# Performance work log

Hardware: AMD Instinct MI355X
Metric: run time of the kernel (lower is better)

The kernel has to match this reference:

```python
import jax, jax.numpy as jnp
import numpy as np

DIM = 512
NUM_LATENTS = 512
HIDDEN = 48  # PointEmbed sinusoidal embedding dim (divisible by 6)


def make_basis():
    k = HIDDEN // 6
    e = (2.0 ** np.arange(k)) * np.pi
    z = np.zeros(k)
    basis = np.stack([
        np.concatenate([e, z, z]),
        np.concatenate([z, e, z]),
        np.concatenate([z, z, e]),
    ])  # [3, HIDDEN//2]
    return jnp.asarray(basis, jnp.float32)


def layernorm(x, g, b, eps=1e-5):
    m = x.mean(-1, keepdims=True)
    v = ((x - m) ** 2).mean(-1, keepdims=True)
    return (x - m) / jnp.sqrt(v + eps) * g + b


def point_embed(x, basis, w, b):
    # x: [B, N, 3] -> [B, N, DIM//2]
    proj = jnp.einsum('bnd,de->bne', x, basis)
    feat = jnp.concatenate([jnp.sin(proj), jnp.cos(proj), x], axis=-1)  # [B,N,51]
    return feat @ w + b


def fps_single(points, num_samples):
    # deterministic farthest point sampling starting at index 0; non-differentiable
    pts = jax.lax.stop_gradient(points)
    N = pts.shape[0]

    def body(carry, _):
        dists, last = carry
        d = jnp.sum((pts - pts[last]) ** 2, axis=-1)
        dists = jnp.minimum(dists, d)
        nxt = jnp.argmax(dists).astype(jnp.int32)
        return (dists, nxt), nxt

    init = (jnp.full((N,), 1e10, pts.dtype), jnp.int32(0))
    _, idxs = jax.lax.scan(body, init, None, length=num_samples - 1)
    return jnp.concatenate([jnp.zeros((1,), jnp.int32), idxs])


def setup_inputs() -> dict:
    key = jax.random.key(0)
    ks = jax.random.split(key, 16)
    B, T, N, D = 16, 3, 2048, 3
    s = 0.02
    inp = {
        'pc': jax.random.normal(ks[0], (B, T, N, D), jnp.float32),
        'pc2': jax.random.normal(ks[1], (B, T, N, D), jnp.float32),
        'basis': make_basis(),
        'pe_w': jax.random.normal(ks[2], (HIDDEN + 3, DIM // 2), jnp.float32) * s,
        'pe_b': jnp.zeros((DIM // 2,), jnp.float32),
        'lnq_g': jnp.ones((DIM,), jnp.float32), 'lnq_b': jnp.zeros((DIM,), jnp.float32),
        'lnc_g': jnp.ones((DIM,), jnp.float32), 'lnc_b': jnp.zeros((DIM,), jnp.float32),
        'wq': jax.random.normal(ks[3], (DIM, DIM), jnp.float32) * s,
        'wkv': jax.random.normal(ks[4], (DIM, 2 * DIM), jnp.float32) * s,
        'wo': jax.random.normal(ks[5], (DIM, DIM), jnp.float32) * s,
        'bo': jnp.zeros((DIM,), jnp.float32),
        'lnf_g': jnp.ones((DIM,), jnp.float32), 'lnf_b': jnp.zeros((DIM,), jnp.float32),
        'w1': jax.random.normal(ks[6], (DIM, 8 * DIM), jnp.float32) * s,
        'b1': jnp.zeros((8 * DIM,), jnp.float32),
        'w2': jax.random.normal(ks[7], (4 * DIM, DIM), jnp.float32) * s,
        'b2': jnp.zeros((DIM,), jnp.float32),
    }
    return inp


def reference(pc, pc2, basis, pe_w, pe_b, lnq_g, lnq_b, lnc_g, lnc_b,
              wq, wkv, wo, bo, lnf_g, lnf_b, w1, b1, w2, b2):
    B, T, N, D = pc.shape
    # FPS on the first frame, per batch element (batch-local indices)
    idx = jax.vmap(lambda p: fps_single(p, NUM_LATENTS))(pc[:, 0])  # [B, M]
    idx4 = idx[:, None, :, None]  # broadcast over T and D
    sampled = jnp.take_along_axis(pc, idx4, axis=2).reshape(B * T, NUM_LATENTS, D)
    sampled2 = jnp.take_along_axis(pc2, idx4, axis=2).reshape(B * T, NUM_LATENTS, D)
    pcf = pc.reshape(B * T, N, D)
    pcf2 = pc2.reshape(B * T, N, D)

    emb_s = jnp.concatenate([point_embed(sampled, basis, pe_w, pe_b),
                             point_embed(sampled2, basis, pe_w, pe_b)], axis=-1)
    emb_c = jnp.concatenate([point_embed(pcf, basis, pe_w, pe_b),
                             point_embed(pcf2, basis, pe_w, pe_b)], axis=-1)

    # PreNorm cross-attention (1 head, dim_head = DIM)
    q_in = layernorm(emb_s, lnq_g, lnq_b)
    c_in = layernorm(emb_c, lnc_g, lnc_b)
    q = q_in @ wq
    kv = c_in @ wkv
    k, v = jnp.split(kv, 2, axis=-1)
    scale = DIM ** -0.5
    attn = jax.nn.softmax(jnp.einsum('bmd,bnd->bmn', q, k) * scale, axis=-1)
    out = jnp.einsum('bmn,bnd->bmd', attn, v) @ wo + bo
    x = out + emb_s

    # PreNorm GEGLU feed-forward
    h = layernorm(x, lnf_g, lnf_b) @ w1 + b1
    a, g = jnp.split(h, 2, axis=-1)
    x = (a * jax.nn.gelu(g, approximate=False)) @ w2 + b2 + x

    return x.reshape(B, T, NUM_LATENTS, DIM)
```

## Files before the change

kernel.cpp:

```cpp
#include <hip/hip_runtime.h>

#define NB    16
#define NT    3
#define NCTX  2048
#define NLAT  512
#define DIMV  512
#define HALFD 256
#define NFEAT 51
#define NBT   48
#define MROWS 24576
#define GRP   6
#define NGRP  8
#define GROWS 12288

typedef unsigned short bfu;
typedef short bf16x8 __attribute__((ext_vector_type(8)));
typedef float f32x4  __attribute__((ext_vector_type(4)));
typedef float f32x2  __attribute__((ext_vector_type(2)));

__device__ __forceinline__ float bf2f(bfu u){ return __uint_as_float(((unsigned int)u) << 16); }
__device__ __forceinline__ bfu f2bf(float f){
  unsigned int u = __float_as_uint(f);
  u += 0x7FFFu + ((u >> 16) & 1u);
  return (bfu)(u >> 16);
}
__device__ __forceinline__ float loadE(const float* p){ return *p; }
__device__ __forceinline__ float loadE(const bfu* p){ return bf2f(*p); }
__device__ __forceinline__ void storeE(float* p, float v){ *p = v; }
__device__ __forceinline__ void storeE(bfu* p, float v){ *p = f2bf(v); }
__device__ __forceinline__ bfu to_bfu(float f){ return f2bf(f); }
__device__ __forceinline__ bfu to_bfu(bfu u){ return u; }

#define GLD16(gp, lp) __builtin_amdgcn_global_load_lds(                       \
    (const __attribute__((address_space(1))) unsigned int*)(gp),              \
    (__attribute__((address_space(3))) unsigned int*)(lp), 16, 0, 0)

template<int KSTEP>
__device__ __forceinline__ int swzr(int r){
  constexpr int CPR = KSTEP / 8;
  return (KSTEP == 32) ? ((r >> 1) & 3) : (r & (CPR - 1));
}

#define DPP_ARGMAX_STAGE(CTRL)                                                \
  {                                                                           \
    const int svb = __builtin_amdgcn_update_dpp(vb, vb, CTRL, 0xF, 0xF, false); \
    const int sib = __builtin_amdgcn_update_dpp(ib, ib, CTRL, 0xF, 0xF, false); \
    const float sv = __int_as_float(svb);                                     \
    const float cv = __int_as_float(vb);                                      \
    if (sv > cv || (sv == cv && sib < ib)){ vb = svb; ib = sib; }             \
  }

__global__ __attribute__((amdgpu_waves_per_eu(1, 1)))
__launch_bounds__(128) void fps_kernel(const float* __restrict__ pc,
                                       int* __restrict__ idx_out){
#pragma clang fp contract(off)
  __shared__ float4 pts[NCTX];
  __shared__ __align__(16) int mbuf[2][4];
  const int tid = threadIdx.x;
  const int lane = tid & 63, w = tid >> 6;
  const int wbase = w << 10;
  const int b = blockIdx.x;
  const float* src = pc + (size_t)b * (NT * NCTX * 3);

  f32x2 x2[8], y2[8], z2[8], d2[8];
  #pragma unroll
  for (int j = 0; j < 8; ++j){
    #pragma unroll
    for (int h = 0; h < 2; ++h){
      const int p = wbase + ((2 * j + h) << 6) + lane;
      const float xx = src[p * 3 + 0];
      const float yy = src[p * 3 + 1];
      const float zz = src[p * 3 + 2];
      x2[j][h] = xx; y2[j][h] = yy; z2[j][h] = zz;
      pts[p] = make_float4(xx, yy, zz, 0.f);
    }
    d2[j][0] = 1e10f; d2[j][1] = 1e10f;
  }
  if (tid == 0) idx_out[b * NLAT] = 0;
  __syncthreads();

  int last = 0;
  for (int step = 1; step < NLAT; ++step){
    const float4 lp = pts[last];

    #pragma unroll
    for (int j = 0; j < 8; ++j){
      const f32x2 dx = x2[j] - lp.x;
      const f32x2 dy = y2[j] - lp.y;
      const f32x2 dz = z2[j] - lp.z;
      const f32x2 dd = (dx * dx + dy * dy) + dz * dz;
      f32x2 nd;
      nd[0] = fminf(d2[j][0], dd[0]);
      nd[1] = fminf(d2[j][1], dd[1]);
      d2[j] = nd;
    }

    float av[8]; int as_[8];
    #pragma unroll
    for (int j = 0; j < 8; ++j){
      const float lo = d2[j][0], hi = d2[j][1];
      const bool t = hi > lo;
      av[j]  = t ? hi : lo;
      as_[j] = t ? 2 * j + 1 : 2 * j;
    }
    #pragma unroll
    for (int wdt = 4; wdt; wdt >>= 1){
      #pragma unroll
      for (int j = 0; j < wdt; ++j){
        const float lv = av[2 * j], rv = av[2 * j + 1];
        const int   li = as_[2 * j], ri = as_[2 * j + 1];
        const bool t = rv > lv;
        av[j]  = t ? rv : lv;
        as_[j] = t ? ri : li;
      }
    }

    int vb = __float_as_int(av[0]);
    int ib = wbase + (as_[0] << 6) + lane;
    DPP_ARGMAX_STAGE(0x111)
    DPP_ARGMAX_STAGE(0x112)
    DPP_ARGMAX_STAGE(0x114)
    DPP_ARGMAX_STAGE(0x118)
    DPP_ARGMAX_STAGE(0x142)
    DPP_ARGMAX_STAGE(0x143)

    const int par = step & 1;
    if (lane == 63){ mbuf[par][w * 2] = vb; mbuf[par][w * 2 + 1] = ib; }
    __syncthreads();
    const int4 q = *(const int4*)&mbuf[par][0];
    const float f0 = __int_as_float(q.x), f1 = __int_as_float(q.z);
    last = (f1 > f0) ? q.w : q.y;
    if (tid == 0) idx_out[b * NLAT + step] = last;
  }
}

template<bool GATHER, bool WRITE_EMB>
__global__ __launch_bounds__(256) void embed_kernel(
    const float* __restrict__ pc, const float* __restrict__ pc2,
    const int* __restrict__ idx,
    const float* __restrict__ basis, const float* __restrict__ pe_w,
    const float* __restrict__ pe_b,
    const float* __restrict__ ln_g, const float* __restrict__ ln_b,
    bfu* __restrict__ emb, bfu* __restrict__ lnout, int nppbt)
{
  __shared__ float feat[2][16][NFEAT + 1];
  __shared__ float outb[16][DIMV];
  const int tid = threadIdx.x;
  const int p0 = blockIdx.x << 4;

  if (tid < 32){
    const int s = tid >> 4, p = tid & 15;
    const int gp = p0 + p;
    const int bt = gp / nppbt;
    const int n  = gp - bt * nppbt;
    const int bb = bt / NT;
    const int srcn = GATHER ? idx[bb * NLAT + n] : n;
    const float* sp = (s ? pc2 : pc) + ((size_t)bt * NCTX + srcn) * 3;
    const float x0 = sp[0], x1 = sp[1], x2 = sp[2];
    #pragma unroll
    for (int e = 0; e < 24; ++e){
      const float pr = __fadd_rn(__fadd_rn(__fmul_rn(x0, basis[e]),
                                           __fmul_rn(x1, basis[24 + e])),
                                 __fmul_rn(x2, basis[48 + e]));
      feat[s][p][e]      = sinf(pr);
      feat[s][p][24 + e] = cosf(pr);
    }
    feat[s][p][48] = x0; feat[s][p][49] = x1; feat[s][p][50] = x2;
  }
  __syncthreads();

  {
    float w[NFEAT];
    #pragma unroll
    for (int k = 0; k < NFEAT; ++k) w[k] = pe_w[k * HALFD + tid];
    const float bv = pe_b[tid];
    #pragma unroll
    for (int half = 0; half < 2; ++half){
      for (int p = 0; p < 16; ++p){
        float acc = bv;
        #pragma unroll
        for (int k = 0; k < NFEAT; ++k) acc = fmaf(feat[half][p][k], w[k], acc);
        outb[p][half * HALFD + tid] = acc;
      }
    }
  }
  __syncthreads();

  const int lane = tid & 63, wv = tid >> 6;
  for (int pp = 0; pp < 4; ++pp){
    const int p = (wv << 2) + pp;
    const size_t gp = (size_t)p0 + p;
    float x[8];
    #pragma unroll
    for (int j = 0; j < 8; ++j) x[j] = outb[p][lane + (j << 6)];
    float s = 0.f;
    #pragma unroll
    for (int j = 0; j < 8; ++j) s += x[j];
    for (int o = 32; o; o >>= 1) s += __shfl_xor(s, o, 64);
    const float m = s * (1.0f / 512.0f);
    float s2 = 0.f;
    #pragma unroll
    for (int j = 0; j < 8; ++j){ const float d = x[j] - m; s2 = fmaf(d, d, s2); }
    for (int o = 32; o; o >>= 1) s2 += __shfl_xor(s2, o, 64);
    const float inv = 1.0f / sqrtf(s2 * (1.0f / 512.0f) + 1e-5f);
    #pragma unroll
    for (int j = 0; j < 8; ++j){
      const int c = lane + (j << 6);
      const float r = (x[j] - m) * inv * ln_g[c] + ln_b[c];
      const size_t o2 = gp * DIMV + c;
      if (WRITE_EMB) emb[o2] = f2bf(x[j]);
      lnout[o2] = f2bf(r);
    }
  }
}

template<typename TIN>
__global__ __launch_bounds__(256) void transp_kernel(
    const TIN* __restrict__ in, bfu* __restrict__ out, int R, int C,
    long long sIn, long long sOut)
{
  __shared__ bfu t[32][33];
  in  += (size_t)blockIdx.z * sIn;
  out += (size_t)blockIdx.z * sOut;
  const int c0 = blockIdx.x * 32, r0 = blockIdx.y * 32;
  const int tx = threadIdx.x & 31, ty = threadIdx.x >> 5;
  #pragma unroll
  for (int rr = ty; rr < 32; rr += 8)
    t[rr][tx] = to_bfu(in[(size_t)(r0 + rr) * C + c0 + tx]);
  __syncthreads();
  #pragma unroll
  for (int rr = ty; rr < 32; rr += 8)
    out[(size_t)(c0 + rr) * R + r0 + tx] = t[tx][rr];
}

#define EPI_NONE     0
#define EPI_SPLIT    1
#define EPI_SCALE    2
#define EPI_BIAS_RES 3

template<int FH, int KSTEP, typename TC, typename TR, int EPI>
__global__ __launch_bounds__(256, 2) void gemm_mfma(
    const bfu* __restrict__ A, const bfu* __restrict__ B,
    TC* __restrict__ C, TC* __restrict__ C2,
    const float* __restrict__ bias, const TR* __restrict__ res,
    float scale, int N, int K, int lda, int ldb, int ldc,
    long long sA, long long sB, long long sC)
{
  constexpr int BT  = FH * 32;
  constexpr int CPR = KSTEP / 8;
  constexpr int NI  = (BT * CPR) / 256;
  const int bz = blockIdx.z;
  A += (size_t)bz * sA;
  B += (size_t)bz * sB;
  const size_t coff = (size_t)bz * sC;

  __shared__ __align__(16) short As[BT * KSTEP];
  __shared__ __align__(16) short Bs[BT * KSTEP];

  const int tid = threadIdx.x;
  const int lane = tid & 63, w = tid >> 6;
  const int wl = (w << 6) + lane;
  const int m0 = blockIdx.y * BT, n0 = blockIdx.x * BT;
  const int wm = (w & 1) * (FH * 16), wn = (w >> 1) * (FH * 16);
  const int fr = lane & 15, quad = lane >> 4;

  f32x4 acc[FH][FH];
  #pragma unroll
  for (int i = 0; i < FH; ++i)
    #pragma unroll
    for (int j = 0; j < FH; ++j)
      #pragma unroll
      for (int r = 0; r < 4; ++r) acc[i][j][r] = 0.f;

  for (int k0 = 0; k0 < K; k0 += KSTEP){
    #pragma unroll
    for (int i = 0; i < NI; ++i){
      const int ch = i * 256 + wl;
      const int r  = ch / CPR, cs = ch & (CPR - 1);
      const int cg = cs ^ swzr<KSTEP>(r);
      short* la = (short*)As + ((i * 256 + (w << 6)) << 3);
      short* lb = (short*)Bs + ((i * 256 + (w << 6)) << 3);
      GLD16(A + (size_t)(m0 + r) * lda + k0 + cg * 8, la);
      GLD16(B + (size_t)(n0 + r) * ldb + k0 + cg * 8, lb);
    }
    __syncthreads();
    #pragma unroll
    for (int kk = 0; kk < KSTEP / 32; ++kk){
      bf16x8 af[FH], bf[FH];
      #pragma unroll
      for (int i = 0; i < FH; ++i){
        const int row = wm + i * 16 + fr;
        const int cl = (kk * 4 + quad) ^ swzr<KSTEP>(row);
        af[i] = *(const bf16x8*)&As[row * KSTEP + (cl << 3)];
      }
      #pragma unroll
      for (int j = 0; j < FH; ++j){
        const int row = wn + j * 16 + fr;
        const int cl = (kk * 4 + quad) ^ swzr<KSTEP>(row);
        bf[j] = *(const bf16x8*)&Bs[row * KSTEP + (cl << 3)];
      }
      #pragma unroll
      for (int i = 0; i < FH; ++i)
        #pragma unroll
        for (int j = 0; j < FH; ++j)
          acc[i][j] = __builtin_amdgcn_mfma_f32_16x16x32_bf16(af[i], bf[j], acc[i][j], 0, 0, 0);
    }
    __syncthreads();
  }

  TC* Cp = C + coff;
  #pragma unroll
  for (int i = 0; i < FH; ++i){
    #pragma unroll
    for (int r = 0; r < 4; ++r){
      const int cm = m0 + wm + i * 16 + quad * 4 + r;
      #pragma unroll
      for (int j = 0; j < FH; ++j){
        const int cn = n0 + wn + j * 16 + fr;
        float v = acc[i][j][r];
        if (EPI == EPI_SCALE)    v *= scale;
        if (EPI == EPI_BIAS_RES) v = v + bias[cn] + loadE(&res[coff + (size_t)cm * ldc + cn]);
        if (EPI == EPI_SPLIT){
          const int half = N >> 1;
          if (cn < half) storeE(&C [(size_t)cm * half + cn],          v);
          else           storeE(&C2[(size_t)cm * half + (cn - half)], v);
        } else {
          storeE(&Cp[(size_t)cm * ldc + cn], v);
        }
      }
    }
  }
}

__global__ __launch_bounds__(256, 1) void mlp1_mfma(
    const bfu* __restrict__ A, const bfu* __restrict__ B,
    const float* __restrict__ b1, bfu* __restrict__ act)
{
  constexpr int KSTEP = 64, CPR = 8, NI = 4;
  __shared__ __align__(16) short As[128 * KSTEP];
  __shared__ __align__(16) short Ba[128 * KSTEP];
  __shared__ __align__(16) short Bg[128 * KSTEP];

  const int tid = threadIdx.x;
  const int lane = tid & 63, w = tid >> 6;
  const int wl = (w << 6) + lane;
  const int m0 = blockIdx.y * 128, n0 = blockIdx.x * 128;
  const int wm = (w & 1) * 64, wn = (w >> 1) * 64;
  const int fr = lane & 15, quad = lane >> 4;

  f32x4 acca[4][4], accg[4][4];
  #pragma unroll
  for (int i = 0; i < 4; ++i)
    #pragma unroll
    for (int j = 0; j < 4; ++j)
      #pragma unroll
      for (int r = 0; r < 4; ++r){ acca[i][j][r] = 0.f; accg[i][j][r] = 0.f; }

  for (int k0 = 0; k0 < 512; k0 += KSTEP){
    #pragma unroll
    for (int i = 0; i < NI; ++i){
      const int ch = i * 256 + wl;
      const int r  = ch / CPR, cs = ch & (CPR - 1);
      const int cg = cs ^ swzr<KSTEP>(r);
      short* da = (short*)As + ((i * 256 + (w << 6)) << 3);
      short* db = (short*)Ba + ((i * 256 + (w << 6)) << 3);
      short* dg = (short*)Bg + ((i * 256 + (w << 6)) << 3);
      GLD16(A + (size_t)(m0 + r) * 512 + k0 + cg * 8, da);
      GLD16(B + (size_t)(n0 + r) * 512 + k0 + cg * 8, db);
      GLD16(B + (size_t)(n0 + 2048 + r) * 512 + k0 + cg * 8, dg);
    }
    __syncthreads();
    #pragma unroll
    for (int kk = 0; kk < KSTEP / 32; ++kk){
      bf16x8 af[4], ba[4], bg[4];
      #pragma unroll
      for (int i = 0; i < 4; ++i){
        const int row = wm + i * 16 + fr;
        const int cl = (kk * 4 + quad) ^ swzr<KSTEP>(row);
        af[i] = *(const bf16x8*)&As[row * KSTEP + (cl << 3)];
      }
      #pragma unroll
      for (int j = 0; j < 4; ++j){
        const int row = wn + j * 16 + fr;
        const int cl = (kk * 4 + quad) ^ swzr<KSTEP>(row);
        ba[j] = *(const bf16x8*)&Ba[row * KSTEP + (cl << 3)];
        bg[j] = *(const bf16x8*)&Bg[row * KSTEP + (cl << 3)];
      }
      #pragma unroll
      for (int i = 0; i < 4; ++i)
        #pragma unroll
        for (int j = 0; j < 4; ++j){
          acca[i][j] = __builtin_amdgcn_mfma_f32_16x16x32_bf16(af[i], ba[j], acca[i][j], 0, 0, 0);
          accg[i][j] = __builtin_amdgcn_mfma_f32_16x16x32_bf16(af[i], bg[j], accg[i][j], 0, 0, 0);
        }
    }
    __syncthreads();
  }

  #pragma unroll
  for (int i = 0; i < 4; ++i){
    #pragma unroll
    for (int r = 0; r < 4; ++r){
      const int cm = m0 + wm + i * 16 + quad * 4 + r;
      #pragma unroll
      for (int j = 0; j < 4; ++j){
        const int cn = n0 + wn + j * 16 + fr;
        const float a = acca[i][j][r] + b1[cn];
        const float g = accg[i][j][r] + b1[cn + 2048];
        const float ge = g * 0.5f * (1.0f + erff(g * 0.70710678118654752f));
        act[(size_t)cm * 2048 + cn] = f2bf(a * ge);
      }
    }
  }
}

__global__ __launch_bounds__(256) void softmax_kernel(bfu* __restrict__ sc){
  __shared__ float red[4];
  const int tid = threadIdx.x;
  const int lane = tid & 63, wv = tid >> 6;
  bfu* rp = sc + (size_t)blockIdx.x * NCTX;
  float x[8];
  #pragma unroll
  for (int j = 0; j < 8; ++j) x[j] = bf2f(rp[tid + (j << 8)]);
  float mx = x[0];
  #pragma unroll
  for (int j = 1; j < 8; ++j) mx = fmaxf(mx, x[j]);
  for (int o = 32; o; o >>= 1) mx = fmaxf(mx, __shfl_xor(mx, o, 64));
  if (lane == 0) red[wv] = mx;
  __syncthreads();
  mx = fmaxf(fmaxf(red[0], red[1]), fmaxf(red[2], red[3]));
  float sum = 0.f;
  #pragma unroll
  for (int j = 0; j < 8; ++j){ x[j] = __expf(x[j] - mx); sum += x[j]; }
  for (int o = 32; o; o >>= 1) sum += __shfl_xor(sum, o, 64);
  __syncthreads();
  if (lane == 0) red[wv] = sum;
  __syncthreads();
  sum = red[0] + red[1] + red[2] + red[3];
  const float inv = 1.0f / sum;
  #pragma unroll
  for (int j = 0; j < 8; ++j) rp[tid + (j << 8)] = f2bf(x[j] * inv);
}

__global__ __launch_bounds__(256) void ln_kernel(const float* __restrict__ in,
                                                 const float* __restrict__ g,
                                                 const float* __restrict__ b,
                                                 bfu* __restrict__ out){
  const int tid = threadIdx.x, lane = tid & 63, wv = tid >> 6;
  const size_t row = (size_t)blockIdx.x * 4 + wv;
  const float* rp = in + row * DIMV;
  float x[8];
  #pragma unroll
  for (int j = 0; j < 8; ++j) x[j] = rp[lane + (j << 6)];
  float s = 0.f;
  #pragma unroll
  for (int j = 0; j < 8; ++j) s += x[j];
  for (int o = 32; o; o >>= 1) s += __shfl_xor(s, o, 64);
  const float m = s * (1.0f / 512.0f);
  float s2 = 0.f;
  #pragma unroll
  for (int j = 0; j < 8; ++j){ const float d = x[j] - m; s2 = fmaf(d, d, s2); }
  for (int o = 32; o; o >>= 1) s2 += __shfl_xor(s2, o, 64);
  const float inv = 1.0f / sqrtf(s2 * (1.0f / 512.0f) + 1e-5f);
  bfu* op = out + row * DIMV;
  #pragma unroll
  for (int j = 0; j < 8; ++j){
    const int c = lane + (j << 6);
    op[c] = f2bf((x[j] - m) * inv * g[c] + b[c]);
  }
}

extern "C" void kernel_launch(void* const* d_in, const int* in_sizes, int n_in,
                              void* d_out, int out_size, void* d_ws, size_t ws_size,
                              hipStream_t stream)
{
  (void)in_sizes; (void)n_in; (void)out_size;
  if (ws_size < 121667584ull) return;

  const float* pc    = (const float*)d_in[0];
  const float* pc2   = (const float*)d_in[1];
  const float* basis = (const float*)d_in[2];
  const float* pe_w  = (const float*)d_in[3];
  const float* pe_b  = (const float*)d_in[4];
  const float* lnq_g = (const float*)d_in[5];
  const float* lnq_b = (const float*)d_in[6];
  const float* lnc_g = (const float*)d_in[7];
  const float* lnc_b = (const float*)d_in[8];
  const float* wq    = (const float*)d_in[9];
  const float* wkv   = (const float*)d_in[10];
  const float* wo    = (const float*)d_in[11];
  const float* bo    = (const float*)d_in[12];
  const float* lnf_g = (const float*)d_in[13];
  const float* lnf_b = (const float*)d_in[14];
  const float* w1    = (const float*)d_in[15];
  const float* b1    = (const float*)d_in[16];
  const float* w2    = (const float*)d_in[17];
  const float* b2    = (const float*)d_in[18];
  float* xout = (float*)d_out;

  char* ws = (char*)d_ws;
  int* idxb   = (int*)(ws);
  bfu* emb_s  = (bfu*)(ws + 32768);
  bfu* q_in   = (bfu*)(ws + 25198592);
  bfu* c_grp  = (bfu*)(ws + 50364416);
  bfu* k_grp  = (bfu*)(ws + 62947328);
  bfu* v_grp  = (bfu*)(ws + 75530240);
  bfu* qbuf   = (bfu*)(ws + 88113152);
  bfu* wqT    = (bfu*)(ws + 113278976);
  bfu* wkvT   = (bfu*)(ws + 113803264);
  bfu* woT    = (bfu*)(ws + 114851840);
  bfu* w1T    = (bfu*)(ws + 115376128);
  bfu* w2T    = (bfu*)(ws + 119570432);
  bfu* scores  = c_grp;
  bfu* vT      = k_grp;
  bfu* attnout = q_in;
  bfu* lnx     = qbuf;
  bfu* actb    = emb_s;

  transp_kernel<float><<<dim3(16, 16, 1),  256, 0, stream>>>(wq,  wqT,  512,  512, 0, 0);
  transp_kernel<float><<<dim3(32, 16, 1),  256, 0, stream>>>(wkv, wkvT, 512, 1024, 0, 0);
  transp_kernel<float><<<dim3(16, 16, 1),  256, 0, stream>>>(wo,  woT,  512,  512, 0, 0);
  transp_kernel<float><<<dim3(128, 16, 1), 256, 0, stream>>>(w1,  w1T,  512, 4096, 0, 0);
  transp_kernel<float><<<dim3(16, 64, 1),  256, 0, stream>>>(w2,  w2T, 2048,  512, 0, 0);

  fps_kernel<<<NB, 128, 0, stream>>>(pc, idxb);

  embed_kernel<true, true><<<MROWS/16, 256, 0, stream>>>(
      pc, pc2, idxb, basis, pe_w, pe_b, lnq_g, lnq_b, emb_s, q_in, NLAT);

  gemm_mfma<4, 64, bfu, float, EPI_NONE><<<dim3(4, 192, 1), 256, 0, stream>>>(
      q_in, wqT, qbuf, nullptr, nullptr, nullptr, 1.0f,
      512, 512, 512, 512, 512, 0, 0, 0);

  for (int g = 0; g < NGRP; ++g){
    const int bt0 = g * GRP;
    embed_kernel<false, false><<<GROWS/16, 256, 0, stream>>>(
        pc + (size_t)bt0 * NCTX * 3, pc2 + (size_t)bt0 * NCTX * 3, nullptr,
        basis, pe_w, pe_b, lnc_g, lnc_b, nullptr, c_grp, NCTX);

    gemm_mfma<4, 64, bfu, float, EPI_SPLIT><<<dim3(8, 96, 1), 256, 0, stream>>>(
        c_grp, wkvT, k_grp, v_grp, nullptr, nullptr, 1.0f,
        1024, 512, 512, 512, 512, 0, 0, 0);

    gemm_mfma<4, 64, bfu, float, EPI_SCALE><<<dim3(16, 4, GRP), 256, 0, stream>>>(
        qbuf + (size_t)bt0 * 262144, k_grp, scores, nullptr, nullptr, nullptr,
        0.044194173824159216f,
        2048, 512, 512, 512, 2048, 262144, 1048576, 1048576);

    softmax_kernel<<<GRP * 512, 256, 0, stream>>>(scores);

    transp_kernel<bfu><<<dim3(16, 64, GRP), 256, 0, stream>>>(
        v_grp, vT, 2048, 512, 2048*512, 2048*512);

    gemm_mfma<2, 128, bfu, float, EPI_NONE><<<dim3(8, 8, GRP), 256, 0, stream>>>(
        scores, vT, attnout + (size_t)bt0 * 262144, nullptr, nullptr, nullptr, 1.0f,
        512, 2048, 2048, 2048, 512, 1048576, 1048576, 262144);
  }

  gemm_mfma<4, 64, float, bfu, EPI_BIAS_RES><<<dim3(4, 192, 1), 256, 0, stream>>>(
      attnout, woT, xout, nullptr, bo, emb_s, 1.0f,
      512, 512, 512, 512, 512, 0, 0, 0);

  ln_kernel<<<MROWS/4, 256, 0, stream>>>(xout, lnf_g, lnf_b, lnx);

  for (int h = 0; h < 2; ++h){
    const size_t ro = (size_t)h * 12288;
    mlp1_mfma<<<dim3(16, 96, 1), 256, 0, stream>>>(
        lnx + ro * 512, w1T, b1, actb);
    gemm_mfma<4, 64, float, float, EPI_BIAS_RES><<<dim3(4, 96, 1), 256, 0, stream>>>(
        actb, w2T, xout + ro * 512, nullptr, b2, xout + ro * 512, 1.0f,
        512, 2048, 2048, 2048, 512, 0, 0, 0);
  }
}
```

Baseline: 1.747 ms.

## Fuse FPS, first context embed, and weight transposes into one launch

Merges the FPS kernel, the group-0 context embedding and all five weight transposes into a single heterogeneous kernel, using block index to choose the role. The sequential FPS blocks, which use only 16 blocks, now run alongside the embedding and transpose work instead of leaving the GPU idle. Separately, the sin/cos feature computation in the embedding is spread across all 256 threads instead of 32. Risks: waves_per_eu(1,1) applied to the whole fused kernel may limit occupancy for the embed and transpose blocks, and the idle FPS half-block spins on barriers.

```diff
diff --git a/kernel.cpp b/kernel.cpp
--- a/kernel.cpp
+++ b/kernel.cpp
@@ -12,6 +12,7 @@
 #define GRP   6
 #define NGRP  8
 #define GROWS 12288
+#define FUSED_BLKS (NB + GROWS/16 + 4096)
 
 typedef unsigned short bfu;
 typedef short bf16x8 __attribute__((ext_vector_type(8)));
@@ -50,16 +51,11 @@
     if (sv > cv || (sv == cv && sib < ib)){ vb = svb; ib = sib; }             \
   }
 
-__global__ __attribute__((amdgpu_waves_per_eu(1, 1)))
-__launch_bounds__(128) void fps_kernel(const float* __restrict__ pc,
-                                       int* __restrict__ idx_out){
-#pragma clang fp contract(off)
-  __shared__ float4 pts[NCTX];
-  __shared__ __align__(16) int mbuf[2][4];
-  const int tid = threadIdx.x;
+__device__ __forceinline__ void fps_body(int b, int tid, const float* __restrict__ pc,
+                                         int* __restrict__ idx_out,
+                                         float4* pts, int (*mbuf)[4]){
   const int lane = tid & 63, w = tid >> 6;
   const int wbase = w << 10;
-  const int b = blockIdx.x;
   const float* src = pc + (size_t)b * (NT * NCTX * 3);
 
   f32x2 x2[8], y2[8], z2[8], d2[8];
@@ -135,18 +131,17 @@
 }
 
 template<bool GATHER, bool WRITE_EMB>
-__global__ __launch_bounds__(256) void embed_kernel(
+__device__ __forceinline__ void embed_body(
+    int bid, int tid,
     const float* __restrict__ pc, const float* __restrict__ pc2,
     const int* __restrict__ idx,
     const float* __restrict__ basis, const float* __restrict__ pe_w,
     const float* __restrict__ pe_b,
     const float* __restrict__ ln_g, const float* __restrict__ ln_b,
-    bfu* __restrict__ emb, bfu* __restrict__ lnout, int nppbt)
-{
-  __shared__ float feat[2][16][NFEAT + 1];
-  __shared__ float outb[16][DIMV];
-  const int tid = threadIdx.x;
-  const int p0 = blockIdx.x << 4;
+    bfu* __restrict__ emb, bfu* __restrict__ lnout, int nppbt,
+    float (*feat)[16][NFEAT + 1], float (*outb)[DIMV])
+{
+  const int p0 = bid << 4;
 
   if (tid < 32){
     const int s = tid >> 4, p = tid & 15;
@@ -156,16 +151,22 @@
     const int bb = bt / NT;
     const int srcn = GATHER ? idx[bb * NLAT + n] : n;
     const float* sp = (s ? pc2 : pc) + ((size_t)bt * NCTX + srcn) * 3;
-    const float x0 = sp[0], x1 = sp[1], x2 = sp[2];
-    #pragma unroll
-    for (int e = 0; e < 24; ++e){
-      const float pr = __fadd_rn(__fadd_rn(__fmul_rn(x0, basis[e]),
-                                           __fmul_rn(x1, basis[24 + e])),
-                                 __fmul_rn(x2, basis[48 + e]));
-      feat[s][p][e]      = sinf(pr);
-      feat[s][p][24 + e] = cosf(pr);
-    }
-    feat[s][p][48] = x0; feat[s][p][49] = x1; feat[s][p][50] = x2;
+    feat[s][p][48] = sp[0]; feat[s][p][49] = sp[1]; feat[s][p][50] = sp[2];
+  }
+  __syncthreads();
+
+  #pragma unroll
+  for (int t = 0; t < 3; ++t){
+    const int wk  = tid * 3 + t;
+    const int spq = wk / 24;
+    const int e   = wk - spq * 24;
+    const int s = spq >> 4, p = spq & 15;
+    const float x0 = feat[s][p][48], x1 = feat[s][p][49], x2 = feat[s][p][50];
+    const float pr = __fadd_rn(__fadd_rn(__fmul_rn(x0, basis[e]),
+                                         __fmul_rn(x1, basis[24 + e])),
+                               __fmul_rn(x2, basis[48 + e]));
+    feat[s][p][e]      = sinf(pr);
+    feat[s][p][24 + e] = cosf(pr);
   }
   __syncthreads();
 
@@ -214,23 +215,94 @@
   }
 }
 
+template<bool GATHER, bool WRITE_EMB>
+__global__ __launch_bounds__(256) void embed_kernel(
+    const float* __restrict__ pc, const float* __restrict__ pc2,
+    const int* __restrict__ idx,
+    const float* __restrict__ basis, const float* __restrict__ pe_w,
+    const float* __restrict__ pe_b,
+    const float* __restrict__ ln_g, const float* __restrict__ ln_b,
+    bfu* __restrict__ emb, bfu* __restrict__ lnout, int nppbt)
+{
+  __shared__ float feat[2][16][NFEAT + 1];
+  __shared__ float outb[16][DIMV];
+  embed_body<GATHER, WRITE_EMB>(blockIdx.x, threadIdx.x, pc, pc2, idx, basis,
+      pe_w, pe_b, ln_g, ln_b, emb, lnout, nppbt, feat, outb);
+}
+
+template<typename TIN>
+__device__ __forceinline__ void transp_body(
+    const TIN* __restrict__ in, bfu* __restrict__ out, int R, int C,
+    int bx, int by, bfu (*t)[33])
+{
+  const int c0 = bx * 32, r0 = by * 32;
+  const int tx = threadIdx.x & 31, ty = threadIdx.x >> 5;
+  #pragma unroll
+  for (int rr = ty; rr < 32; rr += 8)
+    t[rr][tx] = to_bfu(in[(size_t)(r0 + rr) * C + c0 + tx]);
+  __syncthreads();
+  #pragma unroll
+  for (int rr = ty; rr < 32; rr += 8)
+    out[(size_t)(c0 + rr) * R + r0 + tx] = t[tx][rr];
+}
+
 template<typename TIN>
 __global__ __launch_bounds__(256) void transp_kernel(
     const TIN* __restrict__ in, bfu* __restrict__ out, int R, int C,
     long long sIn, long long sOut)
 {
   __shared__ bfu t[32][33];
-  in  += (size_t)blockIdx.z * sIn;
-  out += (size_t)blockIdx.z * sOut;
-  const int c0 = blockIdx.x * 32, r0 = blockIdx.y * 32;
-  const int tx = threadIdx.x & 31, ty = threadIdx.x >> 5;
-  #pragma unroll
-  for (int rr = ty; rr < 32; rr += 8)
-    t[rr][tx] = to_bfu(in[(size_t)(r0 + rr) * C + c0 + tx]);
-  __syncthreads();
-  #pragma unroll
-  for (int rr = ty; rr < 32; rr += 8)
-    out[(size_t)(c0 + rr) * R + r0 + tx] = t[tx][rr];
+  transp_body<TIN>(in + (size_t)blockIdx.z * sIn, out + (size_t)blockIdx.z * sOut,
+                   R, C, blockIdx.x, blockIdx.y, t);
+}
+
+__global__ __attribute__((amdgpu_waves_per_eu(1, 1)))
+__launch_bounds__(256) void fused_pre(
+    const float* __restrict__ pc, const float* __restrict__ pc2,
+    int* __restrict__ idx_out,
+    const float* __restrict__ basis, const float* __restrict__ pe_w,
+    const float* __restrict__ pe_b,
+    const float* __restrict__ lnc_g, const float* __restrict__ lnc_b,
+    bfu* __restrict__ c_grp,
+    const float* __restrict__ wq, const float* __restrict__ wkv,
+    const float* __restrict__ wo, const float* __restrict__ w1,
+    const float* __restrict__ w2,
+    bfu* __restrict__ wqT, bfu* __restrict__ wkvT, bfu* __restrict__ woT,
+    bfu* __restrict__ w1T, bfu* __restrict__ w2T)
+{
+  __shared__ __align__(16) char smem[39424];
+  const int bid = blockIdx.x, tid = threadIdx.x;
+
+  if (bid < NB){
+    #pragma clang fp contract(off)
+    float4* pts = (float4*)smem;
+    int (*mbuf)[4] = (int(*)[4])(smem + 32768);
+    if (tid < 128){
+      fps_body(bid, tid, pc, idx_out, pts, mbuf);
+    } else {
+      for (int i = 0; i < NLAT; ++i) __syncthreads();
+    }
+    return;
+  }
+  const int rb = bid - NB;
+  if (rb < GROWS / 16){
+    embed_body<false, false>(rb, tid, pc, pc2, nullptr, basis, pe_w, pe_b,
+                             lnc_g, lnc_b, nullptr, c_grp, NCTX,
+                             (float(*)[16][NFEAT + 1])smem,
+                             (float(*)[DIMV])(smem + 6656));
+    return;
+  }
+  int tb = rb - GROWS / 16;
+  bfu (*tile)[33] = (bfu(*)[33])smem;
+  if (tb < 256){ transp_body<float>(wq,  wqT,  512,  512, tb & 15,  tb >> 4, tile); return; }
+  tb -= 256;
+  if (tb < 512){ transp_body<float>(wkv, wkvT, 512, 1024, tb & 31,  tb >> 5, tile); return; }
+  tb -= 512;
+  if (tb < 256){ transp_body<float>(wo,  woT,  512,  512, tb & 15,  tb >> 4, tile); return; }
+  tb -= 256;
+  if (tb < 2048){ transp_body<float>(w1, w1T,  512, 4096, tb & 127, tb >> 7, tile); return; }
+  tb -= 2048;
+  transp_body<float>(w2, w2T, 2048, 512, tb & 15, tb >> 4, tile);
 }
 
 #define EPI_NONE     0
@@ -517,13 +589,9 @@
   bfu* lnx     = qbuf;
   bfu* actb    = emb_s;
 
-  transp_kernel<float><<<dim3(16, 16, 1),  256, 0, stream>>>(wq,  wqT,  512,  512, 0, 0);
-  transp_kernel<float><<<dim3(32, 16, 1),  256, 0, stream>>>(wkv, wkvT, 512, 1024, 0, 0);
-  transp_kernel<float><<<dim3(16, 16, 1),  256, 0, stream>>>(wo,  woT,  512,  512, 0, 0);
-  transp_kernel<float><<<dim3(128, 16, 1), 256, 0, stream>>>(w1,  w1T,  512, 4096, 0, 0);
-  transp_kernel<float><<<dim3(16, 64, 1),  256, 0, stream>>>(w2,  w2T, 2048,  512, 0, 0);
-
-  fps_kernel<<<NB, 128, 0, stream>>>(pc, idxb);
+  fused_pre<<<FUSED_BLKS, 256, 0, stream>>>(
+      pc, pc2, idxb, basis, pe_w, pe_b, lnc_g, lnc_b, c_grp,
+      wq, wkv, wo, w1, w2, wqT, wkvT, woT, w1T, w2T);
 
   embed_kernel<true, true><<<MROWS/16, 256, 0, stream>>>(
       pc, pc2, idxb, basis, pe_w, pe_b, lnq_g, lnq_b, emb_s, q_in, NLAT);
@@ -534,9 +602,11 @@
 
   for (int g = 0; g < NGRP; ++g){
     const int bt0 = g * GRP;
-    embed_kernel<false, false><<<GROWS/16, 256, 0, stream>>>(
-        pc + (size_t)bt0 * NCTX * 3, pc2 + (size_t)bt0 * NCTX * 3, nullptr,
-        basis, pe_w, pe_b, lnc_g, lnc_b, nullptr, c_grp, NCTX);
+    if (g > 0){
+      embed_kernel<false, false><<<GROWS/16, 256, 0, stream>>>(
+          pc + (size_t)bt0 * NCTX * 3, pc2 + (size_t)bt0 * NCTX * 3, nullptr,
+          basis, pe_w, pe_b, lnc_g, lnc_b, nullptr, c_grp, NCTX);
+    }
 
     gemm_mfma<4, 64, bfu, float, EPI_SPLIT><<<dim3(8, 96, 1), 256, 0, stream>>>(
         c_grp, wkvT, k_grp, v_grp, nullptr, nullptr, 1.0f,
```

Result: faster. 1.703 ms (-2.5%).
